# Kernel optimization log

Hardware: AMD Instinct MI355X
Metric: run time of the kernel (lower is better)

Reference implementation:

```python
import jax, jax.numpy as jnp
import numpy as np

N = 50000
E = 800000
IN_C = 128
HID = 64
HEADS = 4
NUM_CLASSES = 10
NUM_GRAPHS = 64
EPS = 1e-5
NEG_SLOPE = 0.2


def setup_inputs() -> dict:
    key = jax.random.key(0)
    ks = jax.random.split(key, 32)
    inp = {}
    inp["x"] = jax.random.normal(ks[0], (N, IN_C), dtype=jnp.float32)
    inp["edge_index"] = jax.random.randint(ks[1], (2, E), 0, N, dtype=jnp.int32)
    inp["batch"] = jnp.sort(jax.random.randint(ks[2], (N,), 0, NUM_GRAPHS, dtype=jnp.int32))
    s = 0.05
    # GATConv1: in=128 -> heads=4, hid=64, concat -> 256
    inp["W1"] = jax.random.normal(ks[3], (IN_C, HEADS * HID), dtype=jnp.float32) * s
    inp["a_src1"] = jax.random.normal(ks[4], (HEADS, HID), dtype=jnp.float32) * s
    inp["a_dst1"] = jax.random.normal(ks[5], (HEADS, HID), dtype=jnp.float32) * s
    inp["b1"] = jnp.zeros((HEADS * HID,), dtype=jnp.float32)
    inp["g1"] = jnp.ones((HEADS * HID,), dtype=jnp.float32)
    inp["be1"] = jnp.zeros((HEADS * HID,), dtype=jnp.float32)
    # GATConv2: in=256 -> heads=4, hid=64, concat -> 256
    inp["W2"] = jax.random.normal(ks[6], (HEADS * HID, HEADS * HID), dtype=jnp.float32) * s
    inp["a_src2"] = jax.random.normal(ks[7], (HEADS, HID), dtype=jnp.float32) * s
    inp["a_dst2"] = jax.random.normal(ks[8], (HEADS, HID), dtype=jnp.float32) * s
    inp["b2"] = jnp.zeros((HEADS * HID,), dtype=jnp.float32)
    inp["g2"] = jnp.ones((HEADS * HID,), dtype=jnp.float32)
    inp["be2"] = jnp.zeros((HEADS * HID,), dtype=jnp.float32)
    # GATConv3: in=256 -> heads=1, hid=64, mean (concat=False) -> 64
    inp["W3"] = jax.random.normal(ks[9], (HEADS * HID, 1 * HID), dtype=jnp.float32) * s
    inp["a_src3"] = jax.random.normal(ks[10], (1, HID), dtype=jnp.float32) * s
    inp["a_dst3"] = jax.random.normal(ks[11], (1, HID), dtype=jnp.float32) * s
    inp["b3"] = jnp.zeros((HID,), dtype=jnp.float32)
    inp["g3"] = jnp.ones((HID,), dtype=jnp.float32)
    inp["be3"] = jnp.zeros((HID,), dtype=jnp.float32)
    # final classifier
    inp["fcW"] = jax.random.normal(ks[12], (HID, NUM_CLASSES), dtype=jnp.float32) * s
    inp["fcb"] = jnp.zeros((NUM_CLASSES,), dtype=jnp.float32)
    return inp


def gat_conv(x, src, dst, W, a_src, a_dst, b, heads, out_c, concat):
    # Linear transform, split heads: [N, H, C]
    h = (x @ W).reshape(-1, heads, out_c)
    # Per-node attention logits (dot with per-head attention vectors): [N, H]
    as_ = jnp.einsum("nhc,hc->nh", h, a_src)
    ad_ = jnp.einsum("nhc,hc->nh", h, a_dst)
    # Per-edge unnormalized attention (src contributes a_src, dst a_dst)
    e = jax.nn.leaky_relu(as_[src] + ad_[dst], NEG_SLOPE)  # [E, H]
    # Segment softmax over destination node (stable)
    e_max = jax.ops.segment_max(e, dst, num_segments=N)  # [N, H]
    ex = jnp.exp(e - e_max[dst])
    denom = jax.ops.segment_sum(ex, dst, num_segments=N)  # [N, H]
    alpha = ex / denom[dst]  # [E, H]
    # Weighted scatter-aggregate of source features
    msg = h[src] * alpha[:, :, None]  # [E, H, C]
    out = jax.ops.segment_sum(msg, dst, num_segments=N)  # [N, H, C]
    out = out.reshape(-1, heads * out_c) if concat else out.mean(axis=1)
    return out + b


def batch_norm(x, gamma, beta):
    mean = x.mean(axis=0)
    var = x.var(axis=0)
    return (x - mean) * jax.lax.rsqrt(var + EPS) * gamma + beta


def reference(x, edge_index, batch, W1, a_src1, a_dst1, b1, g1, be1,
              W2, a_src2, a_dst2, b2, g2, be2,
              W3, a_src3, a_dst3, b3, g3, be3, fcW, fcb):
    src, dst = edge_index[0], edge_index[1]
    h = jax.nn.relu(gat_conv(x, src, dst, W1, a_src1, a_dst1, b1, HEADS, HID, True))
    h = batch_norm(h, g1, be1)  # dropout = identity (eval)
    h = jax.nn.relu(gat_conv(h, src, dst, W2, a_src2, a_dst2, b2, HEADS, HID, True))
    h = batch_norm(h, g2, be2)
    h = jax.nn.relu(gat_conv(h, src, dst, W3, a_src3, a_dst3, b3, 1, HID, False))
    h = batch_norm(h, g3, be3)
    # global mean pool over graphs
    sums = jax.ops.segment_sum(h, batch, num_segments=NUM_GRAPHS)  # [G, HID]
    counts = jax.ops.segment_sum(jnp.ones((h.shape[0],), h.dtype), batch, num_segments=NUM_GRAPHS)
    pooled = sums / jnp.maximum(counts, 1.0)[:, None]
    return pooled @ fcW + fcb
```

## Files before the change

kernel.cpp:

```cpp
#include <hip/hip_runtime.h>
#include <hip/hip_bf16.h>

#define N_NODES 50000
#define NUM_E   800000
#define EPS_BN  1e-5f
#define NUM_GRAPHS 64

typedef __attribute__((ext_vector_type(8))) short bf16x8;
typedef __attribute__((ext_vector_type(4))) float f32x4;
typedef unsigned short ushort_t;
typedef unsigned int uint_t;

static __device__ __forceinline__ unsigned short f2bf(float f) {
    unsigned int u = __float_as_uint(f);
    u += 0x7fffu + ((u >> 16) & 1u);
    return (unsigned short)(u >> 16);
}
static __device__ __forceinline__ uint_t pkbf(float lo, float hi) {
    __hip_bfloat162 t = __float22bfloat162_rn(make_float2(lo, hi));
    return *(uint_t*)&t;
}
static __device__ __forceinline__ float bflo(uint_t u) { return __uint_as_float(u << 16); }
static __device__ __forceinline__ float bfhi(uint_t u) { return __uint_as_float(u & 0xffff0000u); }

__global__ void hist_kernel(const int* __restrict__ ei, int* __restrict__ deg) {
    int e = blockIdx.x * blockDim.x + threadIdx.x;
    if (e >= NUM_E) return;
    atomicAdd(&deg[ei[NUM_E + e]], 1);
}

__global__ void scan_local_kernel(const int* __restrict__ deg, int* __restrict__ rowptr,
                                  int* __restrict__ bsum) {
    __shared__ int ws[4];
    int b = blockIdx.x, t = threadIdx.x;
    int i = b * 256 + t;
    int lane = t & 63, wv = t >> 6;
    int v = (i < N_NODES) ? deg[i] : 0;
    int incl = v;
#pragma unroll
    for (int off = 1; off < 64; off <<= 1) {
        int u = __shfl_up(incl, off, 64);
        if (lane >= off) incl += u;
    }
    if (lane == 63) ws[wv] = incl;
    __syncthreads();
    if (t == 0) {
        int s = 0;
#pragma unroll
        for (int k = 0; k < 4; ++k) { int x = ws[k]; ws[k] = s; s += x; }
        bsum[b] = s;
    }
    __syncthreads();
    if (i < N_NODES) rowptr[i + 1] = ws[wv] + incl;
}

__global__ void scan_sums_kernel(int* __restrict__ bsum, int nb) {
    __shared__ int ws[4];
    int t = threadIdx.x;
    int lane = t & 63, wv = t >> 6;
    int v = (t < nb) ? bsum[t] : 0;
    int incl = v;
#pragma unroll
    for (int off = 1; off < 64; off <<= 1) {
        int u = __shfl_up(incl, off, 64);
        if (lane >= off) incl += u;
    }
    if (lane == 63) ws[wv] = incl;
    __syncthreads();
    if (t == 0) {
        int s = 0;
#pragma unroll
        for (int k = 0; k < 4; ++k) { int x = ws[k]; ws[k] = s; s += x; }
    }
    __syncthreads();
    if (t < nb) bsum[t] = ws[wv] + incl - v;
}

__global__ void scan_add_kernel(int* __restrict__ rowptr, const int* __restrict__ bsum) {
    int b = blockIdx.x, t = threadIdx.x;
    int i = b * 256 + t;
    if (i < N_NODES) rowptr[i + 1] += bsum[b];
    if (b == 0 && t == 0) rowptr[0] = 0;
}

__global__ void scatter_kernel(const int* __restrict__ ei, const int* __restrict__ rowptr,
                               int* __restrict__ fill, int* __restrict__ srcs) {
    int e = blockIdx.x * blockDim.x + threadIdx.x;
    if (e >= NUM_E) return;
    int dst = ei[NUM_E + e];
    int pos = rowptr[dst] + atomicAdd(&fill[dst], 1);
    srcs[pos] = ei[e];
}

__global__ void prep_w_all(const float* __restrict__ W1, const float* __restrict__ W2,
                           const float* __restrict__ W3, ushort_t* __restrict__ w1t,
                           ushort_t* __restrict__ w2t, ushort_t* __restrict__ w3t) {
    int i = blockIdx.x * blockDim.x + threadIdx.x;
    const int S1 = 128 * 256, S2 = 256 * 256, S3 = 256 * 64;
    if (i < S1) {
        int k = i / 256, n = i % 256;
        w1t[n * 128 + k] = f2bf(W1[i]);
    } else if (i < S1 + S2) {
        int j = i - S1; int k = j / 256, n = j % 256;
        w2t[n * 256 + k] = f2bf(W2[j]);
    } else if (i < S1 + S2 + S3) {
        int j = i - S1 - S2; int k = j / 64, n = j % 64;
        w3t[n * 256 + k] = f2bf(W3[j]);
    }
}

template<int K, int NFULL, int BN, bool ABF16>
__global__ __launch_bounds__(256) void gemm_fused_kernel(const void* __restrict__ Araw,
                                                         const ushort_t* __restrict__ Bt,
                                                         ushort_t* __restrict__ C,
                                                         const float* __restrict__ stats,
                                                         const float* __restrict__ g,
                                                         const float* __restrict__ be,
                                                         const float* __restrict__ a_src,
                                                         const float* __restrict__ a_dst,
                                                         float* __restrict__ as_,
                                                         float* __restrict__ ad_) {
    const int NT = BN / 16;
    const int NG = BN / 64;
    __shared__ __align__(16) ushort_t As[128][40];
    __shared__ __align__(16) ushort_t Bs[BN][40];
    __shared__ __align__(16) ushort_t Cs[4][32][64];
    __shared__ __align__(16) float aff_a[K], aff_b[K];
    __shared__ float asrc_s[BN], adst_s[BN];
    int tid = threadIdx.x;
    int lane = tid & 63, w = tid >> 6;
    int row0 = blockIdx.x * 128, col0 = blockIdx.y * BN;
    int m_l = lane & 15, q = lane >> 4;

    for (int c = tid; c < K; c += 256) {
        float a = 1.f, b = 0.f;
        if (stats) {
            float m = stats[c] * (1.f / N_NODES);
            float var = fmaxf(stats[256 + c] * (1.f / N_NODES) - m * m, 0.f);
            float rs = rsqrtf(var + EPS_BN) * g[c];
            a = rs; b = be[c] - m * rs;
        }
        aff_a[c] = a; aff_b[c] = b;
    }
    if (tid < BN) {
        asrc_s[tid] = a_src[col0 + tid];
        adst_s[tid] = a_dst[col0 + tid];
    }
    __syncthreads();

    f32x4 acc[2][NT];
#pragma unroll
    for (int r = 0; r < 2; ++r)
#pragma unroll
        for (int c = 0; c < NT; ++c) acc[r][c] = (f32x4){0.f, 0.f, 0.f, 0.f};

    int ar = tid >> 1, ako = (tid & 1) * 16;

    for (int k0 = 0; k0 < K; k0 += 32) {
        uint_t ow[8];
        int gr = row0 + ar;
        if constexpr (ABF16) {
            const ushort_t* A = (const ushort_t*)Araw;
            uint4 u0 = make_uint4(0, 0, 0, 0), u1 = make_uint4(0, 0, 0, 0);
            if (gr < N_NODES) {
                const ushort_t* ap = A + (long)gr * K + k0 + ako;
                u0 = *(const uint4*)ap;
                u1 = *(const uint4*)(ap + 8);
            }
            uint_t uu[8] = {u0.x, u0.y, u0.z, u0.w, u1.x, u1.y, u1.z, u1.w};
#pragma unroll
            for (int t = 0; t < 8; ++t) {
                int k = k0 + ako + t * 2;
                float lo = bflo(uu[t]) * aff_a[k] + aff_b[k];
                float hi = bfhi(uu[t]) * aff_a[k + 1] + aff_b[k + 1];
                ow[t] = pkbf(lo, hi);
            }
        } else {
            const float* A = (const float*)Araw;
            float v[16];
#pragma unroll
            for (int t = 0; t < 16; ++t) v[t] = 0.f;
            if (gr < N_NODES) {
                const float* ap = A + (long)gr * K + k0 + ako;
#pragma unroll
                for (int t = 0; t < 4; ++t) {
                    float4 f = *(const float4*)(ap + t * 4);
                    v[t * 4 + 0] = f.x; v[t * 4 + 1] = f.y; v[t * 4 + 2] = f.z; v[t * 4 + 3] = f.w;
                }
            }
#pragma unroll
            for (int t = 0; t < 8; ++t) {
                int k = k0 + ako + t * 2;
                float lo = v[t * 2] * aff_a[k] + aff_b[k];
                float hi = v[t * 2 + 1] * aff_a[k + 1] + aff_b[k + 1];
                ow[t] = pkbf(lo, hi);
            }
        }
        if constexpr (BN == 128) {
            int br = tid >> 1, bko = (tid & 1) * 16;
            const ushort_t* bp = Bt + (long)(col0 + br) * K + k0 + bko;
            uint4 b0 = *(const uint4*)bp;
            uint4 b1 = *(const uint4*)(bp + 8);
            *(uint4*)&As[ar][ako] = make_uint4(ow[0], ow[1], ow[2], ow[3]);
            *(uint4*)&As[ar][ako + 8] = make_uint4(ow[4], ow[5], ow[6], ow[7]);
            *(uint4*)&Bs[br][bko] = b0;
            *(uint4*)&Bs[br][bko + 8] = b1;
        } else {
            int br = tid >> 2, bko = (tid & 3) * 8;
            uint4 bv = *(const uint4*)(Bt + (long)(col0 + br) * K + k0 + bko);
            *(uint4*)&As[ar][ako] = make_uint4(ow[0], ow[1], ow[2], ow[3]);
            *(uint4*)&As[ar][ako + 8] = make_uint4(ow[4], ow[5], ow[6], ow[7]);
            *(uint4*)&Bs[br][bko] = bv;
        }
        __syncthreads();

        bf16x8 af[2];
#pragma unroll
        for (int r = 0; r < 2; ++r)
            af[r] = *(const bf16x8*)&As[w * 32 + r * 16 + m_l][q * 8];
#pragma unroll
        for (int c = 0; c < NT; ++c) {
            bf16x8 bf = *(const bf16x8*)&Bs[c * 16 + m_l][q * 8];
#pragma unroll
            for (int r = 0; r < 2; ++r)
                acc[r][c] = __builtin_amdgcn_mfma_f32_16x16x32_bf16(af[r], bf, acc[r][c], 0, 0, 0);
        }
        __syncthreads();
    }

    const int H = NFULL / 64;
#pragma unroll
    for (int gblk = 0; gblk < NG; ++gblk) {
        int hidx = blockIdx.y * NG + gblk;
        int colg = col0 + gblk * 64;
#pragma unroll
        for (int r = 0; r < 2; ++r)
#pragma unroll
            for (int cc = 0; cc < 4; ++cc)
#pragma unroll
                for (int i = 0; i < 4; ++i)
                    Cs[w][r * 16 + q * 4 + i][cc * 16 + m_l] = f2bf(acc[r][gblk * 4 + cc][i]);
#pragma unroll
        for (int j = 0; j < 4; ++j) {
            int flat = j * 64 + lane;
            int lr = flat >> 3, chg = flat & 7;
            int gr = row0 + w * 32 + lr;
            uint4 u = *(uint4*)&Cs[w][lr][chg * 8];
            float f0 = bflo(u.x), f1 = bfhi(u.x), f2 = bflo(u.y), f3 = bfhi(u.y);
            float f4 = bflo(u.z), f5 = bfhi(u.z), f6 = bflo(u.w), f7 = bfhi(u.w);
            int cb = gblk * 64 + chg * 8;
            float s1 = f0 * asrc_s[cb] + f1 * asrc_s[cb + 1] + f2 * asrc_s[cb + 2] + f3 * asrc_s[cb + 3]
                     + f4 * asrc_s[cb + 4] + f5 * asrc_s[cb + 5] + f6 * asrc_s[cb + 6] + f7 * asrc_s[cb + 7];
            float s2 = f0 * adst_s[cb] + f1 * adst_s[cb + 1] + f2 * adst_s[cb + 2] + f3 * adst_s[cb + 3]
                     + f4 * adst_s[cb + 4] + f5 * adst_s[cb + 5] + f6 * adst_s[cb + 6] + f7 * adst_s[cb + 7];
#pragma unroll
            for (int o = 1; o < 8; o <<= 1) {
                s1 += __shfl_xor(s1, o, 64);
                s2 += __shfl_xor(s2, o, 64);
            }
            if (gr < N_NODES) {
                *(uint4*)(C + (long)gr * NFULL + colg + chg * 8) = u;
                if ((lane & 7) == 0) {
                    as_[gr * H + hidx] = s1;
                    ad_[gr * H + hidx] = s2;
                }
            }
        }
    }
}

__global__ __launch_bounds__(256) void agg4_kernel(const ushort_t* __restrict__ h,
                                                   const float* __restrict__ as_,
                                                   const float* __restrict__ ad_,
                                                   const int* __restrict__ rowptr,
                                                   const int* __restrict__ srcs,
                                                   const float* __restrict__ bias,
                                                   ushort_t* __restrict__ out) {
    __shared__ float alds[4][256];
    int lane = threadIdx.x & 63, w = threadIdx.x >> 6;
    int q = lane >> 4, cl = lane & 15;
    int n = blockIdx.x * 16 + w * 4 + q;
    if (n >= N_NODES) return;
    int start = rowptr[n];
    int deg = rowptr[n + 1] - start;

    float4 adv = *(const float4*)(ad_ + n * 4);
    float ad4[4] = {adv.x, adv.y, adv.z, adv.w};

    float mx[4] = {-1e30f, -1e30f, -1e30f, -1e30f};
    float dn[4] = {0.f, 0.f, 0.f, 0.f};
    int s0reg = 0;
    {
        float vst[4] = {-1e30f, -1e30f, -1e30f, -1e30f};
        if (deg > 0) s0reg = srcs[start + min(cl, deg - 1)];
        if (cl < deg) {
            float4 av = *(const float4*)(as_ + s0reg * 4);
            float vv[4] = {av.x + ad4[0], av.y + ad4[1], av.z + ad4[2], av.w + ad4[3]};
#pragma unroll
            for (int hh = 0; hh < 4; ++hh) {
                float v = vv[hh] > 0.f ? vv[hh] : 0.2f * vv[hh];
                vst[hh] = v; mx[hh] = v; dn[hh] = 1.f;
            }
        }
        *(float4*)&alds[w][lane * 4] = make_float4(vst[0], vst[1], vst[2], vst[3]);
        for (int j = cl + 16; j < deg; j += 16) {
            int s = srcs[start + j];
            float4 av = *(const float4*)(as_ + s * 4);
            float vv[4] = {av.x + ad4[0], av.y + ad4[1], av.z + ad4[2], av.w + ad4[3]};
#pragma unroll
            for (int hh = 0; hh < 4; ++hh) {
                float v = vv[hh] > 0.f ? vv[hh] : 0.2f * vv[hh];
                float mn = fmaxf(mx[hh], v);
                dn[hh] = dn[hh] * __expf(mx[hh] - mn) + __expf(v - mn);
                mx[hh] = mn;
            }
        }
    }
    float mloc[4] = {mx[0], mx[1], mx[2], mx[3]};
#pragma unroll
    for (int off = 1; off < 16; off <<= 1)
#pragma unroll
        for (int hh = 0; hh < 4; ++hh) mx[hh] = fmaxf(mx[hh], __shfl_xor(mx[hh], off, 64));
#pragma unroll
    for (int hh = 0; hh < 4; ++hh) dn[hh] *= __expf(mloc[hh] - mx[hh]);
#pragma unroll
    for (int off = 1; off < 16; off <<= 1)
#pragma unroll
        for (int hh = 0; hh < 4; ++hh) dn[hh] += __shfl_xor(dn[hh], off, 64);
    float inv[4];
#pragma unroll
    for (int hh = 0; hh < 4; ++hh) inv[hh] = dn[hh] > 0.f ? 1.f / dn[hh] : 0.f;

    {
        float4 vv = *(const float4*)&alds[w][lane * 4];
        float4 al;
        al.x = __expf(vv.x - mx[0]) * inv[0];
        al.y = __expf(vv.y - mx[1]) * inv[1];
        al.z = __expf(vv.z - mx[2]) * inv[2];
        al.w = __expf(vv.w - mx[3]) * inv[3];
        *(float4*)&alds[w][lane * 4] = al;
    }

    int hd = cl >> 2;
    float acc[16];
#pragma unroll
    for (int k = 0; k < 16; ++k) acc[k] = 0.f;
    for (int chunk = 0; chunk < deg || chunk == 0; chunk += 16) {
        int s = s0reg;
        if (chunk > 0) {
            int j = chunk + cl;
            float4 al = make_float4(0.f, 0.f, 0.f, 0.f);
            s = srcs[start + min(j, deg - 1)];
            if (j < deg) {
                float4 av = *(const float4*)(as_ + s * 4);
                float vv[4] = {av.x + ad4[0], av.y + ad4[1], av.z + ad4[2], av.w + ad4[3]};
                float a4[4];
#pragma unroll
                for (int hh = 0; hh < 4; ++hh) {
                    float v = vv[hh] > 0.f ? vv[hh] : 0.2f * vv[hh];
                    a4[hh] = __expf(v - mx[hh]) * inv[hh];
                }
                al = make_float4(a4[0], a4[1], a4[2], a4[3]);
            }
            *(float4*)&alds[w][lane * 4] = al;
        }
        int cnt = min(16, deg - chunk);
        if (cnt < 0) cnt = 0;
#pragma unroll 4
        for (int e = 0; e < cnt; ++e) {
            int se = __shfl(s, q * 16 + e, 64);
            float al = alds[w][(q * 16 + e) * 4 + hd];
            const ushort_t* hr = h + (long)se * 256 + cl * 16;
            uint4 u0 = *(const uint4*)hr;
            uint4 u1 = *(const uint4*)(hr + 8);
            acc[0] += al * bflo(u0.x);  acc[1] += al * bfhi(u0.x);
            acc[2] += al * bflo(u0.y);  acc[3] += al * bfhi(u0.y);
            acc[4] += al * bflo(u0.z);  acc[5] += al * bfhi(u0.z);
            acc[6] += al * bflo(u0.w);  acc[7] += al * bfhi(u0.w);
            acc[8] += al * bflo(u1.x);  acc[9] += al * bfhi(u1.x);
            acc[10] += al * bflo(u1.y); acc[11] += al * bfhi(u1.y);
            acc[12] += al * bflo(u1.z); acc[13] += al * bfhi(u1.z);
            acc[14] += al * bflo(u1.w); acc[15] += al * bfhi(u1.w);
        }
        if (deg <= 16) break;
    }
    int c0 = cl * 16;
    uint_t ow[8];
#pragma unroll
    for (int t = 0; t < 8; ++t) {
        float lo = fmaxf(acc[t * 2] + bias[c0 + t * 2], 0.f);
        float hi = fmaxf(acc[t * 2 + 1] + bias[c0 + t * 2 + 1], 0.f);
        ow[t] = pkbf(lo, hi);
    }
    ushort_t* op = out + (long)n * 256 + c0;
    *(uint4*)op = make_uint4(ow[0], ow[1], ow[2], ow[3]);
    *(uint4*)(op + 8) = make_uint4(ow[4], ow[5], ow[6], ow[7]);
}

__global__ __launch_bounds__(256) void agg1_kernel(const ushort_t* __restrict__ h,
                                                   const float* __restrict__ as_,
                                                   const float* __restrict__ ad_,
                                                   const int* __restrict__ rowptr,
                                                   const int* __restrict__ srcs,
                                                   const float* __restrict__ bias,
                                                   ushort_t* __restrict__ out) {
    __shared__ float alds1[4][64];
    int lane = threadIdx.x & 63, w = threadIdx.x >> 6;
    int o = lane >> 3, cl = lane & 7;
    int n = blockIdx.x * 32 + w * 8 + o;
    if (n >= N_NODES) return;
    int start = rowptr[n];
    int deg = rowptr[n + 1] - start;
    float adn = ad_[n];

    float mx = -1e30f, dn = 0.f;
    int s0reg = 0;
    {
        float vst = -1e30f;
        if (deg > 0) s0reg = srcs[start + min(cl, deg - 1)];
        if (cl < deg) {
            float v = as_[s0reg] + adn;
            v = v > 0.f ? v : 0.2f * v;
            vst = v; mx = v; dn = 1.f;
        }
        alds1[w][lane] = vst;
        for (int j = cl + 8; j < deg; j += 8) {
            int s = srcs[start + j];
            float v = as_[s] + adn;
            v = v > 0.f ? v : 0.2f * v;
            float mn = fmaxf(mx, v);
            dn = dn * __expf(mx - mn) + __expf(v - mn);
            mx = mn;
        }
    }
    float mloc = mx;
#pragma unroll
    for (int off = 1; off < 8; off <<= 1) mx = fmaxf(mx, __shfl_xor(mx, off, 64));
    dn *= __expf(mloc - mx);
#pragma unroll
    for (int off = 1; off < 8; off <<= 1) dn += __shfl_xor(dn, off, 64);
    float inv = dn > 0.f ? 1.f / dn : 0.f;

    alds1[w][lane] = __expf(alds1[w][lane] - mx) * inv;

    float acc[8] = {0.f, 0.f, 0.f, 0.f, 0.f, 0.f, 0.f, 0.f};
    for (int chunk = 0; chunk < deg || chunk == 0; chunk += 8) {
        int s = s0reg;
        if (chunk > 0) {
            int j = chunk + cl;
            float al = 0.f;
            s = srcs[start + min(j, deg - 1)];
            if (j < deg) {
                float v = as_[s] + adn;
                v = v > 0.f ? v : 0.2f * v;
                al = __expf(v - mx) * inv;
            }
            alds1[w][lane] = al;
        }
        int cnt = min(8, deg - chunk);
        if (cnt < 0) cnt = 0;
#pragma unroll 4
        for (int e = 0; e < cnt; ++e) {
            int se = __shfl(s, o * 8 + e, 64);
            float al = alds1[w][o * 8 + e];
            const ushort_t* hr = h + (long)se * 64 + cl * 8;
            uint4 u = *(const uint4*)hr;
            acc[0] += al * bflo(u.x); acc[1] += al * bfhi(u.x);
            acc[2] += al * bflo(u.y); acc[3] += al * bfhi(u.y);
            acc[4] += al * bflo(u.z); acc[5] += al * bfhi(u.z);
            acc[6] += al * bflo(u.w); acc[7] += al * bfhi(u.w);
        }
        if (deg <= 8) break;
    }
    int c0 = cl * 8;
    uint_t ow[4];
#pragma unroll
    for (int t = 0; t < 4; ++t) {
        float lo = fmaxf(acc[t * 2] + bias[c0 + t * 2], 0.f);
        float hi = fmaxf(acc[t * 2 + 1] + bias[c0 + t * 2 + 1], 0.f);
        ow[t] = pkbf(lo, hi);
    }
    *(uint4*)(out + (long)n * 64 + c0) = make_uint4(ow[0], ow[1], ow[2], ow[3]);
}

template<int C>
__global__ __launch_bounds__(256) void bn_stats_bf16(const ushort_t* __restrict__ x,
                                                     float* __restrict__ stats) {
    const int GROUPS = C / 8;
    const int RS = 256 / GROUPS;
    int tid = threadIdx.x;
    int cg = tid % GROUPS;
    int rs = tid / GROUPS;
    float s[8], s2[8];
#pragma unroll
    for (int k = 0; k < 8; ++k) { s[k] = 0.f; s2[k] = 0.f; }
    for (int n = blockIdx.x * RS + rs; n < N_NODES; n += gridDim.x * RS) {
        uint4 u = *(const uint4*)(x + (long)n * C + cg * 8);
        float f[8] = {bflo(u.x), bfhi(u.x), bflo(u.y), bfhi(u.y),
                      bflo(u.z), bfhi(u.z), bflo(u.w), bfhi(u.w)};
#pragma unroll
        for (int k = 0; k < 8; ++k) { s[k] += f[k]; s2[k] += f[k] * f[k]; }
    }
    __shared__ float red[256][16];
#pragma unroll
    for (int k = 0; k < 8; ++k) { red[tid][k] = s[k]; red[tid][8 + k] = s2[k]; }
    __syncthreads();
    if (tid < C) {
        int g = tid >> 3, k = tid & 7;
        float a = 0.f, b = 0.f;
        for (int r = 0; r < RS; ++r) {
            a += red[g + r * GROUPS][k];
            b += red[g + r * GROUPS][8 + k];
        }
        atomicAdd(&stats[tid], a);
        atomicAdd(&stats[256 + tid], b);
    }
}

__global__ void batch_offsets_kernel(const int* __restrict__ batch, int* __restrict__ goff) {
    int g = threadIdx.x;
    if (g > NUM_GRAPHS) return;
    int lo = 0, hi = N_NODES;
    while (lo < hi) {
        int mid = (lo + hi) >> 1;
        if (batch[mid] < g) lo = mid + 1; else hi = mid;
    }
    goff[g] = lo;
}

__global__ __launch_bounds__(256) void pool2_kernel(const ushort_t* __restrict__ h,
                                                    const int* __restrict__ goff,
                                                    const float* __restrict__ stats,
                                                    const float* __restrict__ g3,
                                                    const float* __restrict__ be3,
                                                    float* __restrict__ pooled) {
    int g = blockIdx.x;
    int c = threadIdx.x & 63;
    int ty = threadIdx.x >> 6;
    int s = goff[g], e = goff[g + 1];
    float sum = 0.f;
    for (int n = s + ty; n < e; n += 4) sum += bflo((uint_t)h[(long)n * 64 + c]);
    __shared__ float red[4][64];
    red[ty][c] = sum;
    __syncthreads();
    if (ty == 0) {
        float tot = red[0][c] + red[1][c] + red[2][c] + red[3][c];
        float v = tot / fmaxf((float)(e - s), 1.f);
        float m = stats[c] * (1.f / N_NODES);
        float var = fmaxf(stats[256 + c] * (1.f / N_NODES) - m * m, 0.f);
        pooled[g * 64 + c] = (v - m) * rsqrtf(var + EPS_BN) * g3[c] + be3[c];
    }
}

__global__ void fc_kernel(const float* __restrict__ pooled, const float* __restrict__ fcW,
                          const float* __restrict__ fcb, float* __restrict__ out) {
    int i = blockIdx.x * blockDim.x + threadIdx.x;
    if (i >= NUM_GRAPHS * 10) return;
    int g = i / 10, j = i % 10;
    float s = 0.f;
    for (int k = 0; k < 64; ++k) s += pooled[g * 64 + k] * fcW[k * 10 + j];
    out[i] = s + fcb[j];
}

extern "C" void kernel_launch(void* const* d_in, const int* in_sizes, int n_in,
                              void* d_out, int out_size, void* d_ws, size_t ws_size,
                              hipStream_t stream) {
    const float* x      = (const float*)d_in[0];
    const int*   ei     = (const int*)d_in[1];
    const int*   batch  = (const int*)d_in[2];
    const float* W1     = (const float*)d_in[3];
    const float* a_src1 = (const float*)d_in[4];
    const float* a_dst1 = (const float*)d_in[5];
    const float* b1     = (const float*)d_in[6];
    const float* g1     = (const float*)d_in[7];
    const float* be1    = (const float*)d_in[8];
    const float* W2     = (const float*)d_in[9];
    const float* a_src2 = (const float*)d_in[10];
    const float* a_dst2 = (const float*)d_in[11];
    const float* b2     = (const float*)d_in[12];
    const float* g2     = (const float*)d_in[13];
    const float* be2    = (const float*)d_in[14];
    const float* W3     = (const float*)d_in[15];
    const float* a_src3 = (const float*)d_in[16];
    const float* a_dst3 = (const float*)d_in[17];
    const float* b3     = (const float*)d_in[18];
    const float* g3     = (const float*)d_in[19];
    const float* be3    = (const float*)d_in[20];
    const float* fcW    = (const float*)d_in[21];
    const float* fcb    = (const float*)d_in[22];
    float* out = (float*)d_out;

    const size_t N = N_NODES, E = NUM_E;
    ushort_t* hbf    = (ushort_t*)d_ws;
    ushort_t* hagg   = hbf + N * 256;
    ushort_t* w1t    = hagg + N * 256;
    ushort_t* w2t    = w1t + 256 * 128;
    ushort_t* w3t    = w2t + 256 * 256;
    float*    as_    = (float*)(w3t + 64 * 256 + 128);
    float*    ad_    = as_ + N * 4;
    int*      deg    = (int*)(ad_ + N * 4);
    int*      fill   = deg + N;
    float*    statsA = (float*)(fill + N);
    float*    statsB = statsA + 512;
    float*    statsC = statsB + 512;
    int*      rowptr = (int*)(statsC + 512);
    int*      srcs   = rowptr + (N + 1);
    int*      bsum   = srcs + E;
    float*    pooled = (float*)(bsum + 256);
    int*      goff   = (int*)(pooled + 64 * 64);

    const int NB = (N_NODES + 255) / 256;

    hipMemsetAsync(deg, 0, sizeof(int) * (2 * N + 3 * 512), stream);
    hist_kernel<<<(NUM_E + 255) / 256, 256, 0, stream>>>(ei, deg);
    scan_local_kernel<<<NB, 256, 0, stream>>>(deg, rowptr, bsum);
    scan_sums_kernel<<<1, 256, 0, stream>>>(bsum, NB);
    scan_add_kernel<<<NB, 256, 0, stream>>>(rowptr, bsum);
    scatter_kernel<<<(NUM_E + 255) / 256, 256, 0, stream>>>(ei, rowptr, fill, srcs);
    batch_offsets_kernel<<<1, 128, 0, stream>>>(batch, goff);
    prep_w_all<<<(128 * 256 + 256 * 256 + 256 * 64 + 255) / 256, 256, 0, stream>>>(W1, W2, W3, w1t, w2t, w3t);

    const int GB = (N_NODES + 127) / 128;

    gemm_fused_kernel<128, 256, 128, false><<<dim3(GB, 2), 256, 0, stream>>>(
        x, w1t, hbf, nullptr, nullptr, nullptr, a_src1, a_dst1, as_, ad_);
    agg4_kernel<<<(N_NODES + 15) / 16, 256, 0, stream>>>(hbf, as_, ad_, rowptr, srcs, b1, hagg);
    bn_stats_bf16<256><<<128, 256, 0, stream>>>(hagg, statsA);

    gemm_fused_kernel<256, 256, 128, true><<<dim3(GB, 2), 256, 0, stream>>>(
        hagg, w2t, hbf, statsA, g1, be1, a_src2, a_dst2, as_, ad_);
    agg4_kernel<<<(N_NODES + 15) / 16, 256, 0, stream>>>(hbf, as_, ad_, rowptr, srcs, b2, hagg);
    bn_stats_bf16<256><<<128, 256, 0, stream>>>(hagg, statsB);

    gemm_fused_kernel<256, 64, 64, true><<<dim3(GB, 1), 256, 0, stream>>>(
        hagg, w3t, hbf, statsB, g2, be2, a_src3, a_dst3, as_, ad_);
    agg1_kernel<<<(N_NODES + 31) / 32, 256, 0, stream>>>(hbf, as_, ad_, rowptr, srcs, b3, hagg);
    bn_stats_bf16<64><<<128, 256, 0, stream>>>(hagg, statsC);

    pool2_kernel<<<NUM_GRAPHS, 256, 0, stream>>>(hagg, goff, statsC, g3, be3, pooled);
    fc_kernel<<<3, 256, 0, stream>>>(pooled, fcW, fcb, out);
}
```

Before: 514.0 us.

## Merge CSR setup into one cooperative kernel and fuse pooling with classifier

Replaces the memset, histogram, three scan kernels, scatter, batch-offset and weight-prep launches with a single cooperative kernel that uses grid-wide syncs between phases. The same kernel also pre-converts x to bf16, so the first GEMM reads bf16 instead of fp32. The pooling and final FC kernels are merged into one. The aim is to cut launch and inter-kernel gaps, at the cost of grid.sync overheads and a fixed 1024-block grid doing the atomic-heavy phases.

```diff
diff --git a/kernel.cpp b/kernel.cpp
--- a/kernel.cpp
+++ b/kernel.cpp
@@ -1,5 +1,8 @@
 #include <hip/hip_runtime.h>
 #include <hip/hip_bf16.h>
+#include <hip/hip_cooperative_groups.h>
+
+namespace cg = cooperative_groups;
 
 #define N_NODES 50000
 #define NUM_E   800000
@@ -23,94 +26,116 @@
 static __device__ __forceinline__ float bflo(uint_t u) { return __uint_as_float(u << 16); }
 static __device__ __forceinline__ float bfhi(uint_t u) { return __uint_as_float(u & 0xffff0000u); }
 
-__global__ void hist_kernel(const int* __restrict__ ei, int* __restrict__ deg) {
-    int e = blockIdx.x * blockDim.x + threadIdx.x;
-    if (e >= NUM_E) return;
-    atomicAdd(&deg[ei[NUM_E + e]], 1);
-}
-
-__global__ void scan_local_kernel(const int* __restrict__ deg, int* __restrict__ rowptr,
-                                  int* __restrict__ bsum) {
+__global__ void setup_kernel(const int* __restrict__ ei, const int* __restrict__ batch,
+                             const float* __restrict__ x, const float* __restrict__ W1,
+                             const float* __restrict__ W2, const float* __restrict__ W3,
+                             ushort_t* __restrict__ xbf, ushort_t* __restrict__ w1t,
+                             ushort_t* __restrict__ w2t, ushort_t* __restrict__ w3t,
+                             int* __restrict__ deg, float* __restrict__ stats3,
+                             int* __restrict__ rowptr, int* __restrict__ srcs,
+                             int* __restrict__ bsum, int* __restrict__ goff) {
+    cg::grid_group grid = cg::this_grid();
     __shared__ int ws[4];
-    int b = blockIdx.x, t = threadIdx.x;
-    int i = b * 256 + t;
-    int lane = t & 63, wv = t >> 6;
-    int v = (i < N_NODES) ? deg[i] : 0;
-    int incl = v;
-#pragma unroll
-    for (int off = 1; off < 64; off <<= 1) {
-        int u = __shfl_up(incl, off, 64);
-        if (lane >= off) incl += u;
-    }
-    if (lane == 63) ws[wv] = incl;
-    __syncthreads();
-    if (t == 0) {
-        int s = 0;
-#pragma unroll
-        for (int k = 0; k < 4; ++k) { int x = ws[k]; ws[k] = s; s += x; }
-        bsum[b] = s;
-    }
-    __syncthreads();
-    if (i < N_NODES) rowptr[i + 1] = ws[wv] + incl;
-}
-
-__global__ void scan_sums_kernel(int* __restrict__ bsum, int nb) {
-    __shared__ int ws[4];
-    int t = threadIdx.x;
-    int lane = t & 63, wv = t >> 6;
-    int v = (t < nb) ? bsum[t] : 0;
-    int incl = v;
-#pragma unroll
-    for (int off = 1; off < 64; off <<= 1) {
-        int u = __shfl_up(incl, off, 64);
-        if (lane >= off) incl += u;
-    }
-    if (lane == 63) ws[wv] = incl;
-    __syncthreads();
-    if (t == 0) {
-        int s = 0;
-#pragma unroll
-        for (int k = 0; k < 4; ++k) { int x = ws[k]; ws[k] = s; s += x; }
-    }
-    __syncthreads();
-    if (t < nb) bsum[t] = ws[wv] + incl - v;
-}
-
-__global__ void scan_add_kernel(int* __restrict__ rowptr, const int* __restrict__ bsum) {
-    int b = blockIdx.x, t = threadIdx.x;
-    int i = b * 256 + t;
-    if (i < N_NODES) rowptr[i + 1] += bsum[b];
-    if (b == 0 && t == 0) rowptr[0] = 0;
-}
-
-__global__ void scatter_kernel(const int* __restrict__ ei, const int* __restrict__ rowptr,
-                               int* __restrict__ fill, int* __restrict__ srcs) {
-    int e = blockIdx.x * blockDim.x + threadIdx.x;
-    if (e >= NUM_E) return;
-    int dst = ei[NUM_E + e];
-    int pos = rowptr[dst] + atomicAdd(&fill[dst], 1);
-    srcs[pos] = ei[e];
-}
-
-__global__ void prep_w_all(const float* __restrict__ W1, const float* __restrict__ W2,
-                           const float* __restrict__ W3, ushort_t* __restrict__ w1t,
-                           ushort_t* __restrict__ w2t, ushort_t* __restrict__ w3t) {
-    int i = blockIdx.x * blockDim.x + threadIdx.x;
-    const int S1 = 128 * 256, S2 = 256 * 256, S3 = 256 * 64;
-    if (i < S1) {
-        int k = i / 256, n = i % 256;
-        w1t[n * 128 + k] = f2bf(W1[i]);
-    } else if (i < S1 + S2) {
-        int j = i - S1; int k = j / 256, n = j % 256;
-        w2t[n * 256 + k] = f2bf(W2[j]);
-    } else if (i < S1 + S2 + S3) {
-        int j = i - S1 - S2; int k = j / 64, n = j % 64;
-        w3t[n * 256 + k] = f2bf(W3[j]);
-    }
-}
-
-template<int K, int NFULL, int BN, bool ABF16>
-__global__ __launch_bounds__(256) void gemm_fused_kernel(const void* __restrict__ Araw,
+    int t = threadIdx.x, lane = t & 63, wv = t >> 6;
+    int gtid = blockIdx.x * 256 + t;
+    int gsz = gridDim.x * 256;
+    const int NB = (N_NODES + 255) / 256;
+    int* fill = deg + N_NODES;
+
+    for (int i = gtid; i < 2 * N_NODES; i += gsz) deg[i] = 0;
+    for (int i = gtid; i < 3 * 512; i += gsz) stats3[i] = 0.f;
+    {
+        const float4* x4 = (const float4*)x;
+        uint2* xb2 = (uint2*)xbf;
+        for (int i = gtid; i < N_NODES * 128 / 4; i += gsz) {
+            float4 v = x4[i];
+            xb2[i] = make_uint2(pkbf(v.x, v.y), pkbf(v.z, v.w));
+        }
+    }
+    {
+        const int S1 = 128 * 256, S2 = 256 * 256, S3 = 256 * 64;
+        for (int i = gtid; i < S1 + S2 + S3; i += gsz) {
+            if (i < S1) {
+                int k = i / 256, n = i % 256;
+                w1t[n * 128 + k] = f2bf(W1[i]);
+            } else if (i < S1 + S2) {
+                int j = i - S1; int k = j / 256, n = j % 256;
+                w2t[n * 256 + k] = f2bf(W2[j]);
+            } else {
+                int j = i - S1 - S2; int k = j / 64, n = j % 64;
+                w3t[n * 256 + k] = f2bf(W3[j]);
+            }
+        }
+    }
+    if (gtid <= NUM_GRAPHS) {
+        int g = gtid, lo = 0, hi = N_NODES;
+        while (lo < hi) {
+            int mid = (lo + hi) >> 1;
+            if (batch[mid] < g) lo = mid + 1; else hi = mid;
+        }
+        goff[g] = lo;
+    }
+    grid.sync();
+
+    for (int e = gtid; e < NUM_E; e += gsz) atomicAdd(&deg[ei[NUM_E + e]], 1);
+    grid.sync();
+
+    if (blockIdx.x < NB) {
+        int b = blockIdx.x;
+        int i = b * 256 + t;
+        int v = (i < N_NODES) ? deg[i] : 0;
+        int incl = v;
+#pragma unroll
+        for (int off = 1; off < 64; off <<= 1) {
+            int u = __shfl_up(incl, off, 64);
+            if (lane >= off) incl += u;
+        }
+        if (lane == 63) ws[wv] = incl;
+        __syncthreads();
+        if (t == 0) {
+            int s = 0;
+#pragma unroll
+            for (int k = 0; k < 4; ++k) { int xx = ws[k]; ws[k] = s; s += xx; }
+            bsum[b] = s;
+        }
+        __syncthreads();
+        if (i < N_NODES) rowptr[i + 1] = ws[wv] + incl;
+    }
+    grid.sync();
+
+    if (blockIdx.x == 0) {
+        int v = (t < NB) ? bsum[t] : 0;
+        int incl = v;
+#pragma unroll
+        for (int off = 1; off < 64; off <<= 1) {
+            int u = __shfl_up(incl, off, 64);
+            if (lane >= off) incl += u;
+        }
+        if (lane == 63) ws[wv] = incl;
+        __syncthreads();
+        if (t == 0) {
+            int s = 0;
+#pragma unroll
+            for (int k = 0; k < 4; ++k) { int xx = ws[k]; ws[k] = s; s += xx; }
+        }
+        __syncthreads();
+        if (t < NB) bsum[t] = ws[wv] + incl - v;
+        if (t == 0) rowptr[0] = 0;
+    }
+    grid.sync();
+
+    for (int i = gtid; i < N_NODES; i += gsz) rowptr[i + 1] += bsum[i >> 8];
+    grid.sync();
+
+    for (int e = gtid; e < NUM_E; e += gsz) {
+        int dst = ei[NUM_E + e];
+        int pos = rowptr[dst] + atomicAdd(&fill[dst], 1);
+        srcs[pos] = ei[e];
+    }
+}
+
+template<int K, int NFULL, int BN>
+__global__ __launch_bounds__(256) void gemm_fused_kernel(const ushort_t* __restrict__ A,
                                                          const ushort_t* __restrict__ Bt,
                                                          ushort_t* __restrict__ C,
                                                          const float* __restrict__ stats,
@@ -159,42 +184,19 @@
     for (int k0 = 0; k0 < K; k0 += 32) {
         uint_t ow[8];
         int gr = row0 + ar;
-        if constexpr (ABF16) {
-            const ushort_t* A = (const ushort_t*)Araw;
-            uint4 u0 = make_uint4(0, 0, 0, 0), u1 = make_uint4(0, 0, 0, 0);
-            if (gr < N_NODES) {
-                const ushort_t* ap = A + (long)gr * K + k0 + ako;
-                u0 = *(const uint4*)ap;
-                u1 = *(const uint4*)(ap + 8);
-            }
-            uint_t uu[8] = {u0.x, u0.y, u0.z, u0.w, u1.x, u1.y, u1.z, u1.w};
-#pragma unroll
-            for (int t = 0; t < 8; ++t) {
-                int k = k0 + ako + t * 2;
-                float lo = bflo(uu[t]) * aff_a[k] + aff_b[k];
-                float hi = bfhi(uu[t]) * aff_a[k + 1] + aff_b[k + 1];
-                ow[t] = pkbf(lo, hi);
-            }
-        } else {
-            const float* A = (const float*)Araw;
-            float v[16];
-#pragma unroll
-            for (int t = 0; t < 16; ++t) v[t] = 0.f;
-            if (gr < N_NODES) {
-                const float* ap = A + (long)gr * K + k0 + ako;
-#pragma unroll
-                for (int t = 0; t < 4; ++t) {
-                    float4 f = *(const float4*)(ap + t * 4);
-                    v[t * 4 + 0] = f.x; v[t * 4 + 1] = f.y; v[t * 4 + 2] = f.z; v[t * 4 + 3] = f.w;
-                }
-            }
-#pragma unroll
-            for (int t = 0; t < 8; ++t) {
-                int k = k0 + ako + t * 2;
-                float lo = v[t * 2] * aff_a[k] + aff_b[k];
-                float hi = v[t * 2 + 1] * aff_a[k + 1] + aff_b[k + 1];
-                ow[t] = pkbf(lo, hi);
-            }
+        uint4 u0 = make_uint4(0, 0, 0, 0), u1 = make_uint4(0, 0, 0, 0);
+        if (gr < N_NODES) {
+            const ushort_t* ap = A + (long)gr * K + k0 + ako;
+            u0 = *(const uint4*)ap;
+            u1 = *(const uint4*)(ap + 8);
+        }
+        uint_t uu[8] = {u0.x, u0.y, u0.z, u0.w, u1.x, u1.y, u1.z, u1.w};
+#pragma unroll
+        for (int t = 0; t < 8; ++t) {
+            int k = k0 + ako + t * 2;
+            float lo = bflo(uu[t]) * aff_a[k] + aff_b[k];
+            float hi = bfhi(uu[t]) * aff_a[k + 1] + aff_b[k + 1];
+            ow[t] = pkbf(lo, hi);
         }
         if constexpr (BN == 128) {
             int br = tid >> 1, bko = (tid & 1) * 16;
@@ -489,13 +491,13 @@
     const int GROUPS = C / 8;
     const int RS = 256 / GROUPS;
     int tid = threadIdx.x;
-    int cg = tid % GROUPS;
+    int cg_ = tid % GROUPS;
     int rs = tid / GROUPS;
     float s[8], s2[8];
 #pragma unroll
     for (int k = 0; k < 8; ++k) { s[k] = 0.f; s2[k] = 0.f; }
     for (int n = blockIdx.x * RS + rs; n < N_NODES; n += gridDim.x * RS) {
-        uint4 u = *(const uint4*)(x + (long)n * C + cg * 8);
+        uint4 u = *(const uint4*)(x + (long)n * C + cg_ * 8);
         float f[8] = {bflo(u.x), bfhi(u.x), bflo(u.y), bfhi(u.y),
                       bflo(u.z), bfhi(u.z), bflo(u.w), bfhi(u.w)};
 #pragma unroll
@@ -517,23 +519,14 @@
     }
 }
 
-__global__ void batch_offsets_kernel(const int* __restrict__ batch, int* __restrict__ goff) {
-    int g = threadIdx.x;
-    if (g > NUM_GRAPHS) return;
-    int lo = 0, hi = N_NODES;
-    while (lo < hi) {
-        int mid = (lo + hi) >> 1;
-        if (batch[mid] < g) lo = mid + 1; else hi = mid;
-    }
-    goff[g] = lo;
-}
-
-__global__ __launch_bounds__(256) void pool2_kernel(const ushort_t* __restrict__ h,
-                                                    const int* __restrict__ goff,
-                                                    const float* __restrict__ stats,
-                                                    const float* __restrict__ g3,
-                                                    const float* __restrict__ be3,
-                                                    float* __restrict__ pooled) {
+__global__ __launch_bounds__(256) void pool_fc_kernel(const ushort_t* __restrict__ h,
+                                                      const int* __restrict__ goff,
+                                                      const float* __restrict__ stats,
+                                                      const float* __restrict__ g3,
+                                                      const float* __restrict__ be3,
+                                                      const float* __restrict__ fcW,
+                                                      const float* __restrict__ fcb,
+                                                      float* __restrict__ out) {
     int g = blockIdx.x;
     int c = threadIdx.x & 63;
     int ty = threadIdx.x >> 6;
@@ -541,6 +534,7 @@
     float sum = 0.f;
     for (int n = s + ty; n < e; n += 4) sum += bflo((uint_t)h[(long)n * 64 + c]);
     __shared__ float red[4][64];
+    __shared__ float pv[64];
     red[ty][c] = sum;
     __syncthreads();
     if (ty == 0) {
@@ -548,18 +542,16 @@
         float v = tot / fmaxf((float)(e - s), 1.f);
         float m = stats[c] * (1.f / N_NODES);
         float var = fmaxf(stats[256 + c] * (1.f / N_NODES) - m * m, 0.f);
-        pooled[g * 64 + c] = (v - m) * rsqrtf(var + EPS_BN) * g3[c] + be3[c];
-    }
-}
-
-__global__ void fc_kernel(const float* __restrict__ pooled, const float* __restrict__ fcW,
-                          const float* __restrict__ fcb, float* __restrict__ out) {
-    int i = blockIdx.x * blockDim.x + threadIdx.x;
-    if (i >= NUM_GRAPHS * 10) return;
-    int g = i / 10, j = i % 10;
-    float s = 0.f;
-    for (int k = 0; k < 64; ++k) s += pooled[g * 64 + k] * fcW[k * 10 + j];
-    out[i] = s + fcb[j];
+        pv[c] = (v - m) * rsqrtf(var + EPS_BN) * g3[c] + be3[c];
+    }
+    __syncthreads();
+    if (threadIdx.x < 10) {
+        int j = threadIdx.x;
+        float acc = fcb[j];
+#pragma unroll
+        for (int k = 0; k < 64; ++k) acc += pv[k] * fcW[k * 10 + j];
+        out[g * 10 + j] = acc;
+    }
 }
 
 extern "C" void kernel_launch(void* const* d_in, const int* in_sizes, int n_in,
@@ -593,7 +585,8 @@
     const size_t N = N_NODES, E = NUM_E;
     ushort_t* hbf    = (ushort_t*)d_ws;
     ushort_t* hagg   = hbf + N * 256;
-    ushort_t* w1t    = hagg + N * 256;
+    ushort_t* xbf    = hagg + N * 256;
+    ushort_t* w1t    = xbf + N * 128;
     ushort_t* w2t    = w1t + 256 * 128;
     ushort_t* w3t    = w2t + 256 * 256;
     float*    as_    = (float*)(w3t + 64 * 256 + 128);
@@ -606,37 +599,32 @@
     int*      rowptr = (int*)(statsC + 512);
     int*      srcs   = rowptr + (N + 1);
     int*      bsum   = srcs + E;
-    float*    pooled = (float*)(bsum + 256);
-    int*      goff   = (int*)(pooled + 64 * 64);
-
-    const int NB = (N_NODES + 255) / 256;
-
-    hipMemsetAsync(deg, 0, sizeof(int) * (2 * N + 3 * 512), stream);
-    hist_kernel<<<(NUM_E + 255) / 256, 256, 0, stream>>>(ei, deg);
-    scan_local_kernel<<<NB, 256, 0, stream>>>(deg, rowptr, bsum);
-    scan_sums_kernel<<<1, 256, 0, stream>>>(bsum, NB);
-    scan_add_kernel<<<NB, 256, 0, stream>>>(rowptr, bsum);
-    scatter_kernel<<<(NUM_E + 255) / 256, 256, 0, stream>>>(ei, rowptr, fill, srcs);
-    batch_offsets_kernel<<<1, 128, 0, stream>>>(batch, goff);
-    prep_w_all<<<(128 * 256 + 256 * 256 + 256 * 64 + 255) / 256, 256, 0, stream>>>(W1, W2, W3, w1t, w2t, w3t);
+    int*      goff   = bsum + 256;
+
+    {
+        void* args[] = {(void*)&ei, (void*)&batch, (void*)&x, (void*)&W1, (void*)&W2, (void*)&W3,
+                        (void*)&xbf, (void*)&w1t, (void*)&w2t, (void*)&w3t,
+                        (void*)&deg, (void*)&statsA, (void*)&rowptr, (void*)&srcs,
+                        (void*)&bsum, (void*)&goff};
+        hipLaunchCooperativeKernel((void*)setup_kernel, dim3(1024), dim3(256), args, 0, stream);
+    }
 
     const int GB = (N_NODES + 127) / 128;
 
-    gemm_fused_kernel<128, 256, 128, false><<<dim3(GB, 2), 256, 0, stream>>>(
-        x, w1t, hbf, nullptr, nullptr, nullptr, a_src1, a_dst1, as_, ad_);
+    gemm_fused_kernel<128, 256, 128><<<dim3(GB, 2), 256, 0, stream>>>(
+        xbf, w1t, hbf, nullptr, nullptr, nullptr, a_src1, a_dst1, as_, ad_);
     agg4_kernel<<<(N_NODES + 15) / 16, 256, 0, stream>>>(hbf, as_, ad_, rowptr, srcs, b1, hagg);
     bn_stats_bf16<256><<<128, 256, 0, stream>>>(hagg, statsA);
 
-    gemm_fused_kernel<256, 256, 128, true><<<dim3(GB, 2), 256, 0, stream>>>(
+    gemm_fused_kernel<256, 256, 128><<<dim3(GB, 2), 256, 0, stream>>>(
         hagg, w2t, hbf, statsA, g1, be1, a_src2, a_dst2, as_, ad_);
     agg4_kernel<<<(N_NODES + 15) / 16, 256, 0, stream>>>(hbf, as_, ad_, rowptr, srcs, b2, hagg);
     bn_stats_bf16<256><<<128, 256, 0, stream>>>(hagg, statsB);
 
-    gemm_fused_kernel<256, 64, 64, true><<<dim3(GB, 1), 256, 0, stream>>>(
+    gemm_fused_kernel<256, 64, 64><<<dim3(GB, 1), 256, 0, stream>>>(
         hagg, w3t, hbf, statsB, g2, be2, a_src3, a_dst3, as_, ad_);
     agg1_kernel<<<(N_NODES + 31) / 32, 256, 0, stream>>>(hbf, as_, ad_, rowptr, srcs, b3, hagg);
     bn_stats_bf16<64><<<128, 256, 0, stream>>>(hagg, statsC);
 
-    pool2_kernel<<<NUM_GRAPHS, 256, 0, stream>>>(hagg, goff, statsC, g3, be3, pooled);
-    fc_kernel<<<3, 256, 0, stream>>>(pooled, fcW, fcb, out);
-}
+    pool_fc_kernel<<<NUM_GRAPHS, 256, 0, stream>>>(hagg, goff, statsC, g3, be3, fcW, fcb, out);
+}
```

After: 1.024 ms. 1.99x slower.
